# Kernel tuning notes

Hardware: AMD Instinct MI355X
Metric: run time of the kernel (lower is better)

## Reference

```python
import jax, jax.numpy as jnp
import numpy as np

N_TASK = 50000
N_PROC = 256
N_EDGES = 800000
EMB = 64
HEADS = 4
NLAYERS = 3
EDIM = 8
TDIM = 16
PDIM = 8
NGRAPHS = 8


def setup_inputs():
    key = jax.random.key(0)
    ks = jax.random.split(key, 30)

    def nrm(k, shape, fan_in):
        return jax.random.normal(k, shape, jnp.float32) / np.float32(np.sqrt(fan_in))

    inp = {}
    inp["x_task"] = jax.random.normal(ks[0], (N_TASK, TDIM), jnp.float32)
    inp["x_proc"] = jax.random.normal(ks[1], (N_PROC, PDIM), jnp.float32)
    inp["edge_index"] = jax.random.randint(ks[2], (2, N_EDGES), 0, N_TASK, dtype=jnp.int32)
    inp["edge_attr"] = jax.random.uniform(ks[3], (N_EDGES, EDIM), jnp.float32)
    inp["task_batch"] = jnp.sort(jax.random.randint(ks[4], (N_TASK,), 0, NGRAPHS, dtype=jnp.int32))
    inp["proc_batch"] = jnp.sort(jax.random.randint(ks[5], (N_PROC,), 0, NGRAPHS, dtype=jnp.int32))
    # input embeds
    inp["W_task"] = nrm(ks[6], (TDIM, EMB), TDIM)
    inp["b_task"] = jnp.zeros((EMB,), jnp.float32)
    inp["W_proc"] = nrm(ks[7], (PDIM, EMB), PDIM)
    inp["b_proc"] = jnp.zeros((EMB,), jnp.float32)
    # per-layer GAT params (stacked over layers)
    inp["gat_W"] = nrm(ks[8], (NLAYERS, EMB, HEADS * EMB), EMB)
    inp["gat_We"] = nrm(ks[9], (NLAYERS, EDIM, HEADS * EMB), EDIM)
    inp["att_src"] = nrm(ks[10], (NLAYERS, HEADS, EMB), EMB)
    inp["att_dst"] = nrm(ks[11], (NLAYERS, HEADS, EMB), EMB)
    inp["att_edge"] = nrm(ks[12], (NLAYERS, HEADS, EMB), EMB)
    inp["gat_b"] = jnp.zeros((NLAYERS, HEADS * EMB), jnp.float32)
    inp["proj_W"] = nrm(ks[13], (NLAYERS, HEADS * EMB, EMB), HEADS * EMB)
    inp["proj_b"] = jnp.zeros((NLAYERS, EMB), jnp.float32)
    inp["ln_g"] = jnp.ones((NLAYERS, EMB), jnp.float32)
    inp["ln_b"] = jnp.zeros((NLAYERS, EMB), jnp.float32)
    # heads
    inp["pt_W1"] = nrm(ks[14], (EMB, EMB // 2), EMB)
    inp["pt_b1"] = jnp.zeros((EMB // 2,), jnp.float32)
    inp["pt_W2"] = nrm(ks[15], (EMB // 2, 1), EMB // 2)
    inp["pt_b2"] = jnp.zeros((1,), jnp.float32)
    inp["v_W1"] = nrm(ks[16], (2 * EMB, EMB), 2 * EMB)
    inp["v_b1"] = jnp.zeros((EMB,), jnp.float32)
    inp["v_W2"] = nrm(ks[17], (EMB, 1), EMB)
    inp["v_b2"] = jnp.zeros((1,), jnp.float32)
    return inp


def _gat_layer(x, src, dst, eattr, W, We, a_s, a_d, a_e, bias):
    # PyG GATConv(in=-1 shared lin, heads=H, concat=True, edge_dim) with self loops already appended
    n = x.shape[0]
    xl = (x @ W).reshape(n, HEADS, EMB)            # [N,H,D]
    el = (eattr @ We).reshape(-1, HEADS, EMB)      # [E,H,D]
    a_src = jnp.einsum("nhd,hd->nh", xl, a_s)
    a_dst = jnp.einsum("nhd,hd->nh", xl, a_d)
    a_edg = jnp.einsum("ehd,hd->eh", el, a_e)
    alpha = jax.nn.leaky_relu(a_src[src] + a_dst[dst] + a_edg, 0.2)  # [E,H]
    m = jax.ops.segment_max(alpha, dst, num_segments=n)
    ex = jnp.exp(alpha - m[dst])
    denom = jax.ops.segment_sum(ex, dst, num_segments=n)
    coeff = ex / (denom[dst] + 1e-16)
    out = jax.ops.segment_sum(coeff[:, :, None] * xl[src], dst, num_segments=n)
    return out.reshape(n, HEADS * EMB) + bias


def _mean_pool(x, batch, g):
    s = jax.ops.segment_sum(x, batch, num_segments=g)
    cnt = jax.ops.segment_sum(jnp.ones((x.shape[0], 1), x.dtype), batch, num_segments=g)
    return s / jnp.maximum(cnt, 1.0)


def reference(x_task, x_proc, edge_attr, W_task, b_task, W_proc, b_proc, gat_W, gat_We,
              att_src, att_dst, att_edge, gat_b, proj_W, proj_b, ln_g, ln_b,
              pt_W1, pt_b1, pt_W2, pt_b2, v_W1, v_b1, v_W2, v_b2,
              edge_index, task_batch, proc_batch):
    h_t = x_task @ W_task + b_task
    h_p = x_proc @ W_proc + b_proc
    # add self loops; self-loop edge_attr = mean of edge_attr (PyG fill_value='mean')
    loop = jnp.arange(N_TASK, dtype=edge_index.dtype)
    src = jnp.concatenate([edge_index[0], loop])
    dst = jnp.concatenate([edge_index[1], loop])
    ea = jnp.concatenate([edge_attr, jnp.broadcast_to(edge_attr.mean(0), (N_TASK, EDIM))], axis=0)
    for l in range(NLAYERS):
        upd = _gat_layer(h_t, src, dst, ea, gat_W[l], gat_We[l], att_src[l], att_dst[l], att_edge[l], gat_b[l])
        upd = jax.nn.elu(upd @ proj_W[l] + proj_b[l])
        h = h_t + upd
        mu = h.mean(-1, keepdims=True)
        var = ((h - mu) ** 2).mean(-1, keepdims=True)
        h_t = (h - mu) / jnp.sqrt(var + 1e-5) * ln_g[l] + ln_b[l]
    task_logits = (jax.nn.relu(h_t @ pt_W1 + pt_b1) @ pt_W2 + pt_b2)[:, 0]
    tp = _mean_pool(h_t, task_batch, NGRAPHS)
    pp = _mean_pool(h_p, proc_batch, NGRAPHS)
    ge = jnp.concatenate([tp, pp], axis=1)
    value = jax.nn.relu(ge @ v_W1 + v_b1) @ v_W2 + v_b2
    return task_logits, value, h_t, h_p
```

## Files before the change

### kernel.cpp

```cpp
#include <hip/hip_runtime.h>
#include <hip/hip_bf16.h>
#include <math.h>

#define NT 50000
#define NP 256
#define NE 800000
#define ET 850000
#define EMBD 64
#define NHEADS 4
#define HE 256
#define NG 8
#define NBLK 49

typedef __attribute__((ext_vector_type(8))) short bf16x8;
typedef __attribute__((ext_vector_type(4))) float f32x4;

#define OFF_DEG    0u
#define OFF_INDPTR 200192u
#define OFF_CURSOR 400384u
#define OFF_BLKSUM 600576u
#define OFF_MG     600832u
#define OFF_MH     601216u
#define OFF_MEAN   601280u
#define OFF_TPSUM  601344u
#define OFF_TPCNT  603392u
#define OFF_ER0    603648u
#define OFF_ER1    14203648u
#define OFF_ER2    27803648u
#define OFF_ASRC   41403648u
#define OFF_ADST   42204416u
#define OFF_HT     43005184u
#define OFF_XL     55817472u
#define OFF_AGG    81417472u
#define OFF_WXF    107042048u
#define OFF_WPF    107140352u
#define OFF_WSD    107238656u

__device__ __forceinline__ float bf_lo(unsigned int u) {
  union { unsigned int i; float f; } v; v.i = u << 16; return v.f;
}
__device__ __forceinline__ float bf_hi(unsigned int u) {
  union { unsigned int i; float f; } v; v.i = u & 0xffff0000u; return v.f;
}
__device__ __forceinline__ unsigned pk2(float a, float b) {
  unsigned ua = __bfloat16_as_ushort(__float2bfloat16(a));
  unsigned ub = __bfloat16_as_ushort(__float2bfloat16(b));
  return ua | (ub << 16);
}

__global__ __launch_bounds__(256) void k_degree_mean(const int* __restrict__ ei1,
    const float* __restrict__ ea, int* __restrict__ deg, float* __restrict__ sums) {
  __shared__ float lds[256];
  int tid = threadIdx.x;
  int e = blockIdx.x * 256 + tid;
  if (e < ET) {
    int d = (e < NE) ? ei1[e] : (e - NE);
    atomicAdd(&deg[d], 1);
  }
  int k = tid & 7, rl = tid >> 3;
  float s = 0.f;
  for (int row = blockIdx.x * 32 + rl; row < NE; row += gridDim.x * 32)
    s += ea[(size_t)row * 8 + k];
  lds[tid] = s;
  __syncthreads();
  for (int off = 128; off >= 8; off >>= 1) {
    if (tid < off) lds[tid] += lds[tid + off];
    __syncthreads();
  }
  if (tid < 8) atomicAdd(&sums[tid], lds[tid]);
}

__global__ __launch_bounds__(1024) void k_scanA(const int* __restrict__ deg,
    int* __restrict__ indptr, int* __restrict__ blksum) {
  __shared__ int wsum[16];
  int tid = threadIdx.x, lane = tid & 63, wid = tid >> 6;
  int i = blockIdx.x * 1024 + tid;
  int v = (i < NT) ? deg[i] : 0;
  int x = v;
  #pragma unroll
  for (int off = 1; off < 64; off <<= 1) {
    int t = __shfl_up(x, off, 64);
    if (lane >= off) x += t;
  }
  if (lane == 63) wsum[wid] = x;
  __syncthreads();
  if (wid == 0 && lane < 16) {
    int w = wsum[lane];
    #pragma unroll
    for (int off = 1; off < 16; off <<= 1) {
      int t = __shfl_up(w, off, 64);
      if (lane >= off) w += t;
    }
    wsum[lane] = w;
  }
  __syncthreads();
  int woff = (wid == 0) ? 0 : wsum[wid - 1];
  if (i < NT) indptr[i] = x + woff - v;
  if (tid == 1023) blksum[blockIdx.x] = wsum[15];
}

__global__ __launch_bounds__(1024) void k_scanB(const int* __restrict__ blksum,
    int* __restrict__ indptr, int* __restrict__ cursor) {
  __shared__ int bs[NBLK];
  int tid = threadIdx.x;
  if (tid < NBLK) bs[tid] = blksum[tid];
  __syncthreads();
  int off = 0;
  for (int j = 0; j < (int)blockIdx.x; j++) off += bs[j];
  int i = blockIdx.x * 1024 + tid;
  if (i < NT) {
    int e = indptr[i] + off;
    indptr[i] = e;
    cursor[i] = e;
  }
  if (blockIdx.x == 0 && tid == 0) {
    int tot = 0;
    for (int j = 0; j < NBLK; j++) tot += bs[j];
    indptr[NT] = tot;
  }
}

__global__ __launch_bounds__(256) void k_mprep(const float* __restrict__ We,
    const float* __restrict__ ae, const float* __restrict__ msum,
    const float* __restrict__ Wx, const float* __restrict__ as_all,
    const float* __restrict__ ad_all,
    float* __restrict__ Mg, float* __restrict__ Mh, __hip_bfloat16* __restrict__ wsd) {
  int t = threadIdx.x;
  if (t < 96) {
    int l = t >> 5, idx = t & 31, k = idx >> 2, h = idx & 3;
    const float* Wl = We + (size_t)l * 8 * HE;
    const float* al = ae + (size_t)l * NHEADS * EMBD;
    float s = 0.f;
    #pragma unroll
    for (int d = 0; d < 64; d++) s += Wl[k * HE + h * 64 + d] * al[h * 64 + d];
    Mg[t] = s;
  }
  __syncthreads();
  if (t < 12) {
    int l = t >> 2, h = t & 3;
    float m = 0.f;
    #pragma unroll
    for (int k = 0; k < 8; k++) m += msum[k] * (1.f / NE) * Mg[l * 32 + k * 4 + h];
    Mh[t] = m;
  }
  for (int v = t; v < 3072; v += 256) {
    int l = v >> 10, rem = v & 1023;
    int kb = rem >> 9, rem2 = rem & 511;
    int lane = rem2 >> 3, j = rem2 & 7;
    int quad = lane >> 4, l15 = lane & 15;
    int k = kb * 32 + quad * 8 + j;
    float val = 0.f;
    if (l15 < 8) {
      int h = l15 & 3;
      const float* av = ((l15 < 4) ? as_all : ad_all) + (size_t)l * NHEADS * EMBD + h * 64;
      const float* Wr = Wx + (size_t)l * 64 * 256 + (size_t)k * 256 + h * 64;
      #pragma unroll
      for (int d = 0; d < 64; d++) val += Wr[d] * av[d];
    }
    wsd[(size_t)l * 1024 + (size_t)(kb * 64 + lane) * 8 + j] = __float2bfloat16(val);
  }
}

__global__ __launch_bounds__(256) void k_fill(const int* __restrict__ ei0,
    const int* __restrict__ ei1, const float* __restrict__ ea,
    const float* __restrict__ Mg, const float* __restrict__ Mh,
    int* __restrict__ cursor,
    uint4* __restrict__ er0, uint4* __restrict__ er1, uint4* __restrict__ er2) {
  __shared__ float MgS[96];
  __shared__ float MhS[12];
  int t = threadIdx.x;
  if (t < 96) MgS[t] = Mg[t];
  if (t < 12) MhS[t] = Mh[t];
  __syncthreads();
  int e = blockIdx.x * 256 + t;
  if (e >= ET) return;
  int d, s;
  float r[3][4];
  if (e < NE) {
    d = ei1[e]; s = ei0[e];
    const float4* pp = (const float4*)(ea + (size_t)e * 8);
    float4 v0 = pp[0], v1 = pp[1];
    float v[8] = {v0.x, v0.y, v0.z, v0.w, v1.x, v1.y, v1.z, v1.w};
    #pragma unroll
    for (int l = 0; l < 3; l++) {
      #pragma unroll
      for (int h = 0; h < 4; h++) {
        float acc = 0.f;
        #pragma unroll
        for (int k = 0; k < 8; k++) acc += v[k] * MgS[l * 32 + k * 4 + h];
        r[l][h] = acc;
      }
    }
  } else {
    d = e - NE; s = d;
    #pragma unroll
    for (int l = 0; l < 3; l++)
      #pragma unroll
      for (int h = 0; h < 4; h++) r[l][h] = MhS[l * 4 + h];
  }
  int p = atomicAdd(&cursor[d], 1);
  uint4 rc;
  rc.x = (unsigned)s; rc.w = 0u;
  rc.y = pk2(r[0][0], r[0][1]); rc.z = pk2(r[0][2], r[0][3]); er0[p] = rc;
  rc.y = pk2(r[1][0], r[1][1]); rc.z = pk2(r[1][2], r[1][3]); er1[p] = rc;
  rc.y = pk2(r[2][0], r[2][1]); rc.z = pk2(r[2][2], r[2][3]); er2[p] = rc;
}

__global__ void k_prep_w(const float* __restrict__ Wx, const float* __restrict__ Wp,
                         __hip_bfloat16* __restrict__ Wxf, __hip_bfloat16* __restrict__ Wpf) {
  int lane = threadIdx.x;
  int bid = blockIdx.x;
  int quad = lane >> 4, l15 = lane & 15;
  if (bid < 96) {
    int l = bid >> 5, rem = bid & 31, t = rem >> 1, kb = rem & 1;
    const float* Wl = Wx + (size_t)l * 64 * 256;
    __hip_bfloat16* out = Wxf + (size_t)l * 16384 + (size_t)((t * 2 + kb) * 64 + lane) * 8;
    #pragma unroll
    for (int j = 0; j < 8; j++)
      out[j] = __float2bfloat16(Wl[(kb * 32 + quad * 8 + j) * 256 + t * 16 + l15]);
  } else {
    bid -= 96;
    int l = bid >> 5, rem = bid & 31, t = rem >> 3, kb = rem & 7;
    const float* Wl = Wp + (size_t)l * 256 * 64;
    __hip_bfloat16* out = Wpf + (size_t)l * 16384 + (size_t)((t * 8 + kb) * 64 + lane) * 8;
    #pragma unroll
    for (int j = 0; j < 8; j++)
      out[j] = __float2bfloat16(Wl[(kb * 32 + quad * 8 + j) * 64 + t * 16 + l15]);
  }
}

__global__ __launch_bounds__(256) void k_embed_xl(const float* __restrict__ x,
    const float* __restrict__ W, const float* __restrict__ b,
    const __hip_bfloat16* __restrict__ Wf, const __hip_bfloat16* __restrict__ wsd,
    float* __restrict__ ht, __hip_bfloat16* __restrict__ xl,
    float* __restrict__ a_src, float* __restrict__ a_dst) {
  __shared__ __hip_bfloat16 hbuf[64 * 72];
  __shared__ __hip_bfloat16 cb16[64 * 264];
  int tid = threadIdx.x, lane = tid & 63, wave = tid >> 6;
  int quad = lane >> 4, l15 = lane & 15;
  int r0 = blockIdx.x * 64;
  {
    float breg[16];
    #pragma unroll
    for (int k = 0; k < 16; k++) breg[k] = W[k * 64 + lane];
    float bias = b[lane];
    #pragma unroll 1
    for (int rr = 0; rr < 16; rr++) {
      int row = r0 + wave * 16 + rr;
      float acc = bias;
      if (row < NT) {
        const float4* xr = (const float4*)(x + (size_t)row * 16);
        #pragma unroll
        for (int q = 0; q < 4; q++) {
          float4 v = xr[q];
          acc += v.x * breg[q*4+0] + v.y * breg[q*4+1] + v.z * breg[q*4+2] + v.w * breg[q*4+3];
        }
        ht[(size_t)row * 64 + lane] = acc;
      }
      hbuf[(wave * 16 + rr) * 72 + lane] = __float2bfloat16(acc);
    }
  }
  __syncthreads();
  f32x4 acc[16], accE;
  #pragma unroll
  for (int t = 0; t < 16; t++) acc[t] = (f32x4){0.f, 0.f, 0.f, 0.f};
  accE = (f32x4){0.f, 0.f, 0.f, 0.f};
  #pragma unroll
  for (int kb = 0; kb < 2; kb++) {
    bf16x8 a = *(const bf16x8*)(&hbuf[(wave * 16 + l15) * 72 + kb * 32 + quad * 8]);
    #pragma unroll
    for (int t = 0; t < 16; t++) {
      bf16x8 bfr = *(const bf16x8*)(Wf + (size_t)((t * 2 + kb) * 64 + lane) * 8);
      acc[t] = __builtin_amdgcn_mfma_f32_16x16x32_bf16(a, bfr, acc[t], 0, 0, 0);
    }
    bf16x8 bs = *(const bf16x8*)(wsd + (size_t)(kb * 64 + lane) * 8);
    accE = __builtin_amdgcn_mfma_f32_16x16x32_bf16(a, bs, accE, 0, 0, 0);
  }
  int rloc = wave * 16 + quad * 4;
  #pragma unroll
  for (int t = 0; t < 16; t++) {
    #pragma unroll
    for (int reg = 0; reg < 4; reg++)
      cb16[(rloc + reg) * 264 + t * 16 + l15] = __float2bfloat16(acc[t][reg]);
  }
  #pragma unroll
  for (int reg = 0; reg < 4; reg++) {
    int row = r0 + rloc + reg;
    if (l15 < 8 && row < NT) {
      float* dst = (l15 < 4) ? a_src : a_dst;
      dst[row * 4 + (l15 & 3)] = accE[reg];
    }
  }
  __syncthreads();
  #pragma unroll
  for (int k = 0; k < 8; k++) {
    int c = k * 256 + tid;
    int row = c >> 5, off = c & 31;
    if (r0 + row < NT) {
      uint4 v = *(const uint4*)(&cb16[row * 264 + off * 8]);
      *(uint4*)(xl + (size_t)(r0 + row) * HE + off * 8) = v;
    }
  }
}

__global__ __launch_bounds__(256) void k_attn(
    const __hip_bfloat16* __restrict__ xl, const float* __restrict__ a_src,
    const float* __restrict__ a_dst, const uint4* __restrict__ er,
    const int* __restrict__ indptr, const float* __restrict__ gb,
    __hip_bfloat16* __restrict__ agg) {
  int node = blockIdx.x * 4 + (threadIdx.x >> 6);
  int lane = threadIdx.x & 63;
  int h = lane >> 4;
  int hbase = lane & 48;
  int e15 = lane & 15;
  int beg = indptr[node], end = indptr[node + 1];
  float adh = a_dst[node * 4 + h];
  float M = -1e30f, S = 0.f;
  float acc0 = 0.f, acc1 = 0.f, acc2 = 0.f, acc3 = 0.f;
  for (int base = beg; base < end; base += 16) {
    int cnt = min(16, end - base);
    bool ok = e15 < cnt;
    uint4 rec; rec.x = 0u; rec.y = 0u; rec.z = 0u; rec.w = 0u;
    if (ok) rec = er[base + e15];
    int my_src = (int)rec.x;
    unsigned wsel = (h < 2) ? rec.y : rec.z;
    float aeh = (h & 1) ? bf_hi(wsel) : bf_lo(wsel);
    float asr = ok ? a_src[(size_t)my_src * 4 + h] : 0.f;
    float al = asr + adh + aeh;
    al = (al > 0.f) ? al : 0.2f * al;
    if (!ok) al = -1e30f;
    float cm = al;
    #pragma unroll
    for (int off = 1; off < 16; off <<= 1) cm = fmaxf(cm, __shfl_xor(cm, off, 64));
    float newM = fmaxf(M, cm);
    float corr = __expf(M - newM);
    float ex = __expf(al - newM);
    float cs = ex;
    #pragma unroll
    for (int off = 1; off < 16; off <<= 1) cs += __shfl_xor(cs, off, 64);
    S = S * corr + cs;
    M = newM;
    acc0 *= corr; acc1 *= corr; acc2 *= corr; acc3 *= corr;
    if (cnt == 16) {
      #pragma unroll 4
      for (int j = 0; j < 16; j++) {
        int src = __shfl(my_src, j, 64);
        float cf = __shfl(ex, hbase | j, 64);
        uint2 u = *(const uint2*)(xl + (size_t)src * HE + lane * 4);
        acc0 += cf * bf_lo(u.x);
        acc1 += cf * bf_hi(u.x);
        acc2 += cf * bf_lo(u.y);
        acc3 += cf * bf_hi(u.y);
      }
    } else {
      for (int j = 0; j < cnt; j++) {
        int src = __shfl(my_src, j, 64);
        float cf = __shfl(ex, hbase | j, 64);
        uint2 u = *(const uint2*)(xl + (size_t)src * HE + lane * 4);
        acc0 += cf * bf_lo(u.x);
        acc1 += cf * bf_hi(u.x);
        acc2 += cf * bf_lo(u.y);
        acc3 += cf * bf_hi(u.y);
      }
    }
  }
  float inv = 1.f / (S + 1e-16f);
  float4 g4 = *(const float4*)(gb + lane * 4);
  unsigned int o0 = __bfloat16_as_ushort(__float2bfloat16(acc0 * inv + g4.x));
  unsigned int o1 = __bfloat16_as_ushort(__float2bfloat16(acc1 * inv + g4.y));
  unsigned int o2 = __bfloat16_as_ushort(__float2bfloat16(acc2 * inv + g4.z));
  unsigned int o3 = __bfloat16_as_ushort(__float2bfloat16(acc3 * inv + g4.w));
  uint2 out; out.x = o0 | (o1 << 16); out.y = o2 | (o3 << 16);
  *(uint2*)(agg + (size_t)node * HE + lane * 4) = out;
}

__global__ __launch_bounds__(256) void k_proj_xl(
    const __hip_bfloat16* __restrict__ agg, const __hip_bfloat16* __restrict__ Wpf,
    const float* __restrict__ pb, const float* __restrict__ g, const float* __restrict__ bln,
    const float* __restrict__ ht_io,
    const __hip_bfloat16* __restrict__ Wxf, const __hip_bfloat16* __restrict__ wsd,
    float* __restrict__ ht_out, __hip_bfloat16* __restrict__ xl,
    float* __restrict__ a_src, float* __restrict__ a_dst) {
  __shared__ __hip_bfloat16 cb16[64 * 264];
  __shared__ __hip_bfloat16 hbuf[64 * 72];
  __shared__ float pbL[64], gL[64], bL[64];
  float* cbf = (float*)cb16;
  int tid = threadIdx.x, lane = tid & 63, wave = tid >> 6;
  int quad = lane >> 4, l15 = lane & 15;
  if (tid < 64) { pbL[tid] = pb[tid]; gL[tid] = g[tid]; bL[tid] = bln[tid]; }
  int r0 = blockIdx.x * 64;
  int arow = r0 + wave * 16 + l15;
  {
    f32x4 pacc[4];
    #pragma unroll
    for (int t = 0; t < 4; t++) pacc[t] = (f32x4){0.f, 0.f, 0.f, 0.f};
    #pragma unroll
    for (int kb = 0; kb < 8; kb++) {
      bf16x8 a = *(const bf16x8*)(agg + (size_t)arow * HE + kb * 32 + quad * 8);
      #pragma unroll
      for (int t = 0; t < 4; t++) {
        bf16x8 bfr = *(const bf16x8*)(Wpf + (size_t)((t * 8 + kb) * 64 + lane) * 8);
        pacc[t] = __builtin_amdgcn_mfma_f32_16x16x32_bf16(a, bfr, pacc[t], 0, 0, 0);
      }
    }
    int rloc = wave * 16 + quad * 4;
    #pragma unroll
    for (int t = 0; t < 4; t++) {
      #pragma unroll
      for (int reg = 0; reg < 4; reg++)
        cbf[(rloc + reg) * 68 + t * 16 + l15] = pacc[t][reg];
    }
  }
  __syncthreads();
  {
    int r = tid >> 2, q = tid & 3;
    int row = r0 + r;
    float h[16], s1 = 0.f, s2 = 0.f;
    const float* hin = ht_io + (size_t)row * 64 + q * 16;
    #pragma unroll
    for (int d = 0; d < 16; d++) {
      float u = cbf[r * 68 + q * 16 + d] + pbL[q * 16 + d];
      u = (u > 0.f) ? u : (__expf(u) - 1.f);
      float hv = hin[d] + u;
      h[d] = hv;
      s1 += hv; s2 += hv * hv;
    }
    s1 += __shfl_xor(s1, 1, 64); s1 += __shfl_xor(s1, 2, 64);
    s2 += __shfl_xor(s2, 1, 64); s2 += __shfl_xor(s2, 2, 64);
    float mu = s1 * 0.015625f;
    float var = s2 * 0.015625f - mu * mu;
    float rstd = rsqrtf(var + 1e-5f);
    float o[16];
    #pragma unroll
    for (int d = 0; d < 16; d++)
      o[d] = (h[d] - mu) * rstd * gL[q * 16 + d] + bL[q * 16 + d];
    if (row < NT) {
      float* outp = ht_out + (size_t)row * 64 + q * 16;
      #pragma unroll
      for (int d4 = 0; d4 < 4; d4++) {
        float4 v; v.x = o[d4*4]; v.y = o[d4*4+1]; v.z = o[d4*4+2]; v.w = o[d4*4+3];
        *(float4*)(outp + d4 * 4) = v;
      }
    }
    uint4 u0, u1;
    u0.x = pk2(o[0], o[1]);  u0.y = pk2(o[2], o[3]);
    u0.z = pk2(o[4], o[5]);  u0.w = pk2(o[6], o[7]);
    u1.x = pk2(o[8], o[9]);  u1.y = pk2(o[10], o[11]);
    u1.z = pk2(o[12], o[13]); u1.w = pk2(o[14], o[15]);
    uint4* hb = (uint4*)(&hbuf[r * 72 + q * 16]);
    hb[0] = u0; hb[1] = u1;
  }
  __syncthreads();
  f32x4 acc[16], accE;
  #pragma unroll
  for (int t = 0; t < 16; t++) acc[t] = (f32x4){0.f, 0.f, 0.f, 0.f};
  accE = (f32x4){0.f, 0.f, 0.f, 0.f};
  #pragma unroll
  for (int kb = 0; kb < 2; kb++) {
    bf16x8 a = *(const bf16x8*)(&hbuf[(wave * 16 + l15) * 72 + kb * 32 + quad * 8]);
    #pragma unroll
    for (int t = 0; t < 16; t++) {
      bf16x8 bfr = *(const bf16x8*)(Wxf + (size_t)((t * 2 + kb) * 64 + lane) * 8);
      acc[t] = __builtin_amdgcn_mfma_f32_16x16x32_bf16(a, bfr, acc[t], 0, 0, 0);
    }
    bf16x8 bs = *(const bf16x8*)(wsd + (size_t)(kb * 64 + lane) * 8);
    accE = __builtin_amdgcn_mfma_f32_16x16x32_bf16(a, bs, accE, 0, 0, 0);
  }
  int rloc = wave * 16 + quad * 4;
  #pragma unroll
  for (int t = 0; t < 16; t++) {
    #pragma unroll
    for (int reg = 0; reg < 4; reg++)
      cb16[(rloc + reg) * 264 + t * 16 + l15] = __float2bfloat16(acc[t][reg]);
  }
  #pragma unroll
  for (int reg = 0; reg < 4; reg++) {
    int row = r0 + rloc + reg;
    if (l15 < 8 && row < NT) {
      float* dst = (l15 < 4) ? a_src : a_dst;
      dst[row * 4 + (l15 & 3)] = accE[reg];
    }
  }
  __syncthreads();
  #pragma unroll
  for (int k = 0; k < 8; k++) {
    int c = k * 256 + tid;
    int row = c >> 5, off = c & 31;
    if (r0 + row < NT) {
      uint4 v = *(const uint4*)(&cb16[row * 264 + off * 8]);
      *(uint4*)(xl + (size_t)(r0 + row) * HE + off * 8) = v;
    }
  }
}

__global__ __launch_bounds__(256) void k_proj_last(
    const __hip_bfloat16* __restrict__ agg, const __hip_bfloat16* __restrict__ Wpf,
    const float* __restrict__ pb, const float* __restrict__ g, const float* __restrict__ bln,
    const float* __restrict__ ht_in, float* __restrict__ ht_out) {
  __shared__ float cbf[64 * 68];
  __shared__ float pbL[64], gL[64], bL[64];
  int tid = threadIdx.x, lane = tid & 63, wave = tid >> 6;
  int quad = lane >> 4, l15 = lane & 15;
  if (tid < 64) { pbL[tid] = pb[tid]; gL[tid] = g[tid]; bL[tid] = bln[tid]; }
  int r0 = blockIdx.x * 64;
  int arow = r0 + wave * 16 + l15;
  f32x4 pacc[4];
  #pragma unroll
  for (int t = 0; t < 4; t++) pacc[t] = (f32x4){0.f, 0.f, 0.f, 0.f};
  #pragma unroll
  for (int kb = 0; kb < 8; kb++) {
    bf16x8 a = *(const bf16x8*)(agg + (size_t)arow * HE + kb * 32 + quad * 8);
    #pragma unroll
    for (int t = 0; t < 4; t++) {
      bf16x8 bfr = *(const bf16x8*)(Wpf + (size_t)((t * 8 + kb) * 64 + lane) * 8);
      pacc[t] = __builtin_amdgcn_mfma_f32_16x16x32_bf16(a, bfr, pacc[t], 0, 0, 0);
    }
  }
  int rloc = wave * 16 + quad * 4;
  #pragma unroll
  for (int t = 0; t < 4; t++) {
    #pragma unroll
    for (int reg = 0; reg < 4; reg++)
      cbf[(rloc + reg) * 68 + t * 16 + l15] = pacc[t][reg];
  }
  __syncthreads();
  int r = tid >> 2, q = tid & 3;
  int row = r0 + r;
  float h[16], s1 = 0.f, s2 = 0.f;
  const float* hin = ht_in + (size_t)row * 64 + q * 16;
  #pragma unroll
  for (int d = 0; d < 16; d++) {
    float u = cbf[r * 68 + q * 16 + d] + pbL[q * 16 + d];
    u = (u > 0.f) ? u : (__expf(u) - 1.f);
    float hv = hin[d] + u;
    h[d] = hv;
    s1 += hv; s2 += hv * hv;
  }
  s1 += __shfl_xor(s1, 1, 64); s1 += __shfl_xor(s1, 2, 64);
  s2 += __shfl_xor(s2, 1, 64); s2 += __shfl_xor(s2, 2, 64);
  float mu = s1 * 0.015625f;
  float var = s2 * 0.015625f - mu * mu;
  float rstd = rsqrtf(var + 1e-5f);
  if (row < NT) {
    float* outp = ht_out + (size_t)row * 64 + q * 16;
    #pragma unroll
    for (int d4 = 0; d4 < 4; d4++) {
      float4 v;
      v.x = (h[d4*4+0] - mu) * rstd * gL[q*16+d4*4+0] + bL[q*16+d4*4+0];
      v.y = (h[d4*4+1] - mu) * rstd * gL[q*16+d4*4+1] + bL[q*16+d4*4+1];
      v.z = (h[d4*4+2] - mu) * rstd * gL[q*16+d4*4+2] + bL[q*16+d4*4+2];
      v.w = (h[d4*4+3] - mu) * rstd * gL[q*16+d4*4+3] + bL[q*16+d4*4+3];
      *(float4*)(outp + d4 * 4) = v;
    }
  }
}

__global__ __launch_bounds__(256) void k_task_head(const float* __restrict__ ht,
    const float* __restrict__ W1, const float* __restrict__ b1,
    const float* __restrict__ W2, const float* __restrict__ b2, float* __restrict__ logits) {
  __shared__ float lh[8 * 64];
  int t = threadIdx.x;
  size_t base = (size_t)blockIdx.x * 8 * 64;
  lh[t] = ht[base + t];
  lh[t + 256] = ht[base + t + 256];
  __syncthreads();
  int i = t >> 5, j = t & 31;
  float s = b1[j];
  #pragma unroll 8
  for (int d = 0; d < 64; d++) s += lh[i * 64 + d] * W1[d * 32 + j];
  s = fmaxf(s, 0.f);
  float p = s * W2[j];
  #pragma unroll
  for (int off = 16; off; off >>= 1) p += __shfl_xor(p, off, 64);
  if (j == 0) logits[blockIdx.x * 8 + i] = p + b2[0];
}

__global__ __launch_bounds__(256) void k_pool_task(const float* __restrict__ ht,
    const int* __restrict__ tb, float* __restrict__ sums, float* __restrict__ cnt) {
  int lane = threadIdx.x & 63, sub = threadIdx.x >> 6;
  float acc[8], c[8];
  #pragma unroll
  for (int g = 0; g < 8; g++) { acc[g] = 0.f; c[g] = 0.f; }
  int lim = min(NT, (int)((blockIdx.x + 1) * 512));
  for (int n = blockIdx.x * 512 + sub; n < lim; n += 4) {
    int g = tb[n];
    float v = ht[(size_t)n * 64 + lane];
    #pragma unroll
    for (int gg = 0; gg < 8; gg++) {
      if (g == gg) { acc[gg] += v; c[gg] += 1.f; }
    }
  }
  #pragma unroll
  for (int g = 0; g < 8; g++) {
    if (__any(acc[g] != 0.f || c[g] != 0.f)) {
      atomicAdd(&sums[g * 64 + lane], acc[g]);
      if (lane == 0) atomicAdd(&cnt[g], c[g]);
    }
  }
}

__global__ __launch_bounds__(512) void k_value(const float* __restrict__ tpsum,
    const float* __restrict__ tpcnt, const float* __restrict__ x_proc,
    const float* __restrict__ W_proc, const float* __restrict__ b_proc,
    float* __restrict__ hp_out, const int* __restrict__ pbatch,
    const float* __restrict__ vW1, const float* __restrict__ vb1,
    const float* __restrict__ vW2, const float* __restrict__ vb2,
    float* __restrict__ val_out) {
  __shared__ float ge[8 * 128];
  int t = threadIdx.x;
  int g = t >> 6, d = t & 63;
  float wreg[8];
  #pragma unroll
  for (int k = 0; k < 8; k++) wreg[k] = W_proc[k * 64 + d];
  float bd = b_proc[d];
  for (int p = g; p < 256; p += 8) {
    const float* xr = x_proc + (size_t)p * 8;
    float a = bd;
    #pragma unroll
    for (int k = 0; k < 8; k++) a += xr[k] * wreg[k];
    hp_out[(size_t)p * 64 + d] = a;
  }
  __syncthreads();
  float c = fmaxf(tpcnt[g], 1.f);
  ge[g * 128 + d] = tpsum[g * 64 + d] / c;
  float s = 0.f, cc = 0.f;
  for (int p = 0; p < 256; p++) {
    int bg = pbatch[p];
    if (bg == g) { s += hp_out[(size_t)p * 64 + d]; cc += 1.f; }
  }
  ge[g * 128 + 64 + d] = s / fmaxf(cc, 1.f);
  __syncthreads();
  float acc = vb1[d];
  #pragma unroll 8
  for (int k = 0; k < 128; k++) acc += ge[g * 128 + k] * vW1[k * 64 + d];
  acc = fmaxf(acc, 0.f);
  float p = acc * vW2[d];
  #pragma unroll
  for (int off = 32; off; off >>= 1) p += __shfl_xor(p, off, 64);
  if (d == 0) val_out[g] = p + vb2[0];
}

extern "C" void kernel_launch(void* const* d_in, const int* in_sizes, int n_in,
                              void* d_out, int out_size, void* d_ws, size_t ws_size,
                              hipStream_t stream) {
  (void)in_sizes; (void)n_in; (void)out_size; (void)ws_size;
  const float* x_task  = (const float*)d_in[0];
  const float* x_proc  = (const float*)d_in[1];
  const int*   eidx    = (const int*)d_in[2];
  const float* eattr   = (const float*)d_in[3];
  const int*   tbatch  = (const int*)d_in[4];
  const int*   pbatch  = (const int*)d_in[5];
  const float* W_task  = (const float*)d_in[6];
  const float* b_task  = (const float*)d_in[7];
  const float* W_proc  = (const float*)d_in[8];
  const float* b_proc  = (const float*)d_in[9];
  const float* gat_W   = (const float*)d_in[10];
  const float* gat_We  = (const float*)d_in[11];
  const float* att_src = (const float*)d_in[12];
  const float* att_dst = (const float*)d_in[13];
  const float* att_edge= (const float*)d_in[14];
  const float* gat_b   = (const float*)d_in[15];
  const float* proj_W  = (const float*)d_in[16];
  const float* proj_b  = (const float*)d_in[17];
  const float* ln_g    = (const float*)d_in[18];
  const float* ln_b    = (const float*)d_in[19];
  const float* pt_W1   = (const float*)d_in[20];
  const float* pt_b1   = (const float*)d_in[21];
  const float* pt_W2   = (const float*)d_in[22];
  const float* pt_b2   = (const float*)d_in[23];
  const float* v_W1    = (const float*)d_in[24];
  const float* v_b1    = (const float*)d_in[25];
  const float* v_W2    = (const float*)d_in[26];
  const float* v_b2    = (const float*)d_in[27];

  char* ws = (char*)d_ws;
  int*   deg    = (int*)(ws + OFF_DEG);
  int*   indptr = (int*)(ws + OFF_INDPTR);
  int*   cursor = (int*)(ws + OFF_CURSOR);
  int*   blksum = (int*)(ws + OFF_BLKSUM);
  float* Mg     = (float*)(ws + OFF_MG);
  float* Mh     = (float*)(ws + OFF_MH);
  float* msum   = (float*)(ws + OFF_MEAN);
  float* tpsum  = (float*)(ws + OFF_TPSUM);
  float* tpcnt  = (float*)(ws + OFF_TPCNT);
  uint4* er0    = (uint4*)(ws + OFF_ER0);
  uint4* er1    = (uint4*)(ws + OFF_ER1);
  uint4* er2    = (uint4*)(ws + OFF_ER2);
  float* a_src  = (float*)(ws + OFF_ASRC);
  float* a_dst  = (float*)(ws + OFF_ADST);
  float* ht     = (float*)(ws + OFF_HT);
  __hip_bfloat16* xl  = (__hip_bfloat16*)(ws + OFF_XL);
  __hip_bfloat16* agg = (__hip_bfloat16*)(ws + OFF_AGG);
  __hip_bfloat16* wxf = (__hip_bfloat16*)(ws + OFF_WXF);
  __hip_bfloat16* wpf = (__hip_bfloat16*)(ws + OFF_WPF);
  __hip_bfloat16* wsd = (__hip_bfloat16*)(ws + OFF_WSD);
  uint4* ers[3] = {er0, er1, er2};

  float* out_logits = (float*)d_out;
  float* out_value  = (float*)d_out + NT;
  float* out_ht     = (float*)d_out + NT + NG;
  float* out_hp     = (float*)d_out + NT + NG + (size_t)NT * EMBD;

  hipMemsetAsync(ws + OFF_DEG, 0, NT * 4, stream);
  hipMemsetAsync(ws + OFF_MEAN, 0, 2144, stream);

  k_degree_mean<<<(ET + 255) / 256, 256, 0, stream>>>(eidx + NE, eattr, deg, msum);
  k_scanA<<<NBLK, 1024, 0, stream>>>(deg, indptr, blksum);
  k_scanB<<<NBLK, 1024, 0, stream>>>(blksum, indptr, cursor);
  k_mprep<<<1, 256, 0, stream>>>(gat_We, att_edge, msum, gat_W, att_src, att_dst,
                                 Mg, Mh, wsd);
  k_prep_w<<<192, 64, 0, stream>>>(gat_W, proj_W, wxf, wpf);
  k_fill<<<(ET + 255) / 256, 256, 0, stream>>>(eidx, eidx + NE, eattr, Mg, Mh,
                                               cursor, er0, er1, er2);
  k_embed_xl<<<782, 256, 0, stream>>>(x_task, W_task, b_task, wxf, wsd,
                                      ht, xl, a_src, a_dst);

  for (int l = 0; l < 3; l++) {
    k_attn<<<NT / 4, 256, 0, stream>>>(xl, a_src, a_dst, ers[l], indptr,
                                       gat_b + l * HE, agg);
    if (l < 2) {
      k_proj_xl<<<782, 256, 0, stream>>>(agg, wpf + (size_t)l * 16384,
                                         proj_b + l * EMBD, ln_g + l * EMBD,
                                         ln_b + l * EMBD, ht,
                                         wxf + (size_t)(l + 1) * 16384,
                                         wsd + (size_t)(l + 1) * 1024,
                                         ht, xl, a_src, a_dst);
    } else {
      k_proj_last<<<782, 256, 0, stream>>>(agg, wpf + (size_t)l * 16384,
                                           proj_b + l * EMBD, ln_g + l * EMBD,
                                           ln_b + l * EMBD, ht, out_ht);
    }
  }

  k_task_head<<<NT / 8, 256, 0, stream>>>(out_ht, pt_W1, pt_b1, pt_W2, pt_b2, out_logits);
  k_pool_task<<<(NT + 511) / 512, 256, 0, stream>>>(out_ht, tbatch, tpsum, tpcnt);
  k_value<<<1, 512, 0, stream>>>(tpsum, tpcnt, x_proc, W_proc, b_proc, out_hp,
                                 pbatch, v_W1, v_b1, v_W2, v_b2, out_value);
}
```

Baseline: 684.7 us.

## Drop online softmax max in GAT attention, batch gathers, fuse pooling into task head

The attention kernel no longer tracks a running maximum with rescaling. It exponentiates the attention logits directly, sums the denominator once at the end, and always handles a full 16-edge chunk, with padded edges weighted zero. Neighbor feature gathers are issued in groups of eight independent loads so more memory requests are in flight, at the cost of extra gathers of row 0 on partial chunks. Mean pooling is folded into the task-head kernel through per-block atomics, which removes one launch but adds many more atomics onto a few hot addresses. Skipping the max subtraction risks overflow if the logits become large.

```diff
diff --git a/kernel.cpp b/kernel.cpp
--- a/kernel.cpp
+++ b/kernel.cpp
@@ -315,10 +315,10 @@
   int e15 = lane & 15;
   int beg = indptr[node], end = indptr[node + 1];
   float adh = a_dst[node * 4 + h];
-  float M = -1e30f, S = 0.f;
+  float S = 0.f;
   float acc0 = 0.f, acc1 = 0.f, acc2 = 0.f, acc3 = 0.f;
   for (int base = beg; base < end; base += 16) {
-    int cnt = min(16, end - base);
+    int cnt = end - base;
     bool ok = e15 < cnt;
     uint4 rec; rec.x = 0u; rec.y = 0u; rec.z = 0u; rec.w = 0u;
     if (ok) rec = er[base + e15];
@@ -328,42 +328,29 @@
     float asr = ok ? a_src[(size_t)my_src * 4 + h] : 0.f;
     float al = asr + adh + aeh;
     al = (al > 0.f) ? al : 0.2f * al;
-    if (!ok) al = -1e30f;
-    float cm = al;
-    #pragma unroll
-    for (int off = 1; off < 16; off <<= 1) cm = fmaxf(cm, __shfl_xor(cm, off, 64));
-    float newM = fmaxf(M, cm);
-    float corr = __expf(M - newM);
-    float ex = __expf(al - newM);
-    float cs = ex;
-    #pragma unroll
-    for (int off = 1; off < 16; off <<= 1) cs += __shfl_xor(cs, off, 64);
-    S = S * corr + cs;
-    M = newM;
-    acc0 *= corr; acc1 *= corr; acc2 *= corr; acc3 *= corr;
-    if (cnt == 16) {
-      #pragma unroll 4
-      for (int j = 0; j < 16; j++) {
-        int src = __shfl(my_src, j, 64);
-        float cf = __shfl(ex, hbase | j, 64);
-        uint2 u = *(const uint2*)(xl + (size_t)src * HE + lane * 4);
-        acc0 += cf * bf_lo(u.x);
-        acc1 += cf * bf_hi(u.x);
-        acc2 += cf * bf_lo(u.y);
-        acc3 += cf * bf_hi(u.y);
+    float ex = ok ? __expf(al) : 0.f;
+    S += ex;
+    #pragma unroll
+    for (int jb = 0; jb < 2; jb++) {
+      int sr[8];
+      #pragma unroll
+      for (int j = 0; j < 8; j++) sr[j] = __shfl(my_src, jb * 8 + j, 64);
+      uint2 u[8];
+      #pragma unroll
+      for (int j = 0; j < 8; j++)
+        u[j] = *(const uint2*)(xl + (size_t)sr[j] * HE + lane * 4);
+      #pragma unroll
+      for (int j = 0; j < 8; j++) {
+        float cf = __shfl(ex, hbase | (jb * 8 + j), 64);
+        acc0 += cf * bf_lo(u[j].x);
+        acc1 += cf * bf_hi(u[j].x);
+        acc2 += cf * bf_lo(u[j].y);
+        acc3 += cf * bf_hi(u[j].y);
       }
-    } else {
-      for (int j = 0; j < cnt; j++) {
-        int src = __shfl(my_src, j, 64);
-        float cf = __shfl(ex, hbase | j, 64);
-        uint2 u = *(const uint2*)(xl + (size_t)src * HE + lane * 4);
-        acc0 += cf * bf_lo(u.x);
-        acc1 += cf * bf_hi(u.x);
-        acc2 += cf * bf_lo(u.y);
-        acc3 += cf * bf_hi(u.y);
-      }
-    }
-  }
+    }
+  }
+  #pragma unroll
+  for (int off = 1; off < 16; off <<= 1) S += __shfl_xor(S, off, 64);
   float inv = 1.f / (S + 1e-16f);
   float4 g4 = *(const float4*)(gb + lane * 4);
   unsigned int o0 = __bfloat16_as_ushort(__float2bfloat16(acc0 * inv + g4.x));
@@ -556,11 +543,14 @@
 }
 
 __global__ __launch_bounds__(256) void k_task_head(const float* __restrict__ ht,
+    const int* __restrict__ tb,
     const float* __restrict__ W1, const float* __restrict__ b1,
-    const float* __restrict__ W2, const float* __restrict__ b2, float* __restrict__ logits) {
+    const float* __restrict__ W2, const float* __restrict__ b2,
+    float* __restrict__ logits, float* __restrict__ sums, float* __restrict__ cnt) {
   __shared__ float lh[8 * 64];
   int t = threadIdx.x;
-  size_t base = (size_t)blockIdx.x * 8 * 64;
+  int row0 = blockIdx.x * 8;
+  size_t base = (size_t)row0 * 64;
   lh[t] = ht[base + t];
   lh[t + 256] = ht[base + t + 256];
   __syncthreads();
@@ -572,29 +562,21 @@
   float p = s * W2[j];
   #pragma unroll
   for (int off = 16; off; off >>= 1) p += __shfl_xor(p, off, 64);
-  if (j == 0) logits[blockIdx.x * 8 + i] = p + b2[0];
-}
-
-__global__ __launch_bounds__(256) void k_pool_task(const float* __restrict__ ht,
-    const int* __restrict__ tb, float* __restrict__ sums, float* __restrict__ cnt) {
-  int lane = threadIdx.x & 63, sub = threadIdx.x >> 6;
-  float acc[8], c[8];
-  #pragma unroll
-  for (int g = 0; g < 8; g++) { acc[g] = 0.f; c[g] = 0.f; }
-  int lim = min(NT, (int)((blockIdx.x + 1) * 512));
-  for (int n = blockIdx.x * 512 + sub; n < lim; n += 4) {
-    int g = tb[n];
-    float v = ht[(size_t)n * 64 + lane];
-    #pragma unroll
-    for (int gg = 0; gg < 8; gg++) {
-      if (g == gg) { acc[gg] += v; c[gg] += 1.f; }
-    }
-  }
-  #pragma unroll
-  for (int g = 0; g < 8; g++) {
-    if (__any(acc[g] != 0.f || c[g] != 0.f)) {
-      atomicAdd(&sums[g * 64 + lane], acc[g]);
-      if (lane == 0) atomicAdd(&cnt[g], c[g]);
+  if (j == 0) logits[row0 + i] = p + b2[0];
+  if (t < 64) {
+    int g0 = tb[row0], g7 = tb[row0 + 7];
+    if (g0 == g7) {
+      float v = 0.f;
+      #pragma unroll
+      for (int r = 0; r < 8; r++) v += lh[r * 64 + t];
+      atomicAdd(&sums[g0 * 64 + t], v);
+      if (t == 0) atomicAdd(&cnt[g0], 8.f);
+    } else {
+      for (int r = 0; r < 8; r++) {
+        int g = tb[row0 + r];
+        atomicAdd(&sums[g * 64 + t], lh[r * 64 + t]);
+        if (t == 0) atomicAdd(&cnt[g], 1.f);
+      }
     }
   }
 }
@@ -732,8 +714,8 @@
     }
   }
 
-  k_task_head<<<NT / 8, 256, 0, stream>>>(out_ht, pt_W1, pt_b1, pt_W2, pt_b2, out_logits);
-  k_pool_task<<<(NT + 511) / 512, 256, 0, stream>>>(out_ht, tbatch, tpsum, tpcnt);
+  k_task_head<<<NT / 8, 256, 0, stream>>>(out_ht, tbatch, pt_W1, pt_b1, pt_W2, pt_b2,
+                                          out_logits, tpsum, tpcnt);
   k_value<<<1, 512, 0, stream>>>(tpsum, tpcnt, x_proc, W_proc, b_proc, out_hp,
                                  pbatch, v_W1, v_b1, v_W2, v_b2, out_value);
 }
```

After: 702.9 us. 1.03x slower.
